# Kernel tuning notes

Measured on AMD Instinct MI355X. Metric: run time of the kernel, lower is better.

## Reference

```python
import jax, jax.numpy as jnp
import numpy as np

B = 64          # graphs per batch
NN = 4096       # nodes per graph (64x64 lattice)
N = B * NN      # total nodes
DEG = 4         # avg degree
E = N * DEG     # total directed edges
DIN, H, L = 1, 128, 64


def setup_inputs() -> dict:
    key = jax.random.key(0)
    ks = jax.random.split(key, 16)
    x = jax.random.normal(ks[0], (N, DIN), dtype=jnp.float32)
    eps = jax.random.normal(ks[1], (B, L), dtype=jnp.float32)
    # per-graph random edges, offset so they never cross graphs
    src = jax.random.randint(ks[2], (E,), 0, NN)
    dst = jax.random.randint(ks[3], (E,), 0, NN)
    off = (jnp.arange(E) // (NN * DEG)) * NN
    edge_index = jnp.stack([src + off, dst + off]).astype(jnp.int32)
    batch = (jnp.arange(N) // NN).astype(jnp.int32)
    s = 0.02
    p = lambda k, shp: s * jax.random.normal(k, shp, dtype=jnp.float32)
    return {
        "x": x, "eps": eps,
        "enc_w1": p(ks[4], (DIN, H)), "enc_b1": jnp.zeros((H,), jnp.float32),
        "enc_w2": p(ks[5], (H, H)),   "enc_b2": jnp.zeros((H,), jnp.float32),
        "mu_w": p(ks[6], (H, L)),     "mu_b": jnp.zeros((L,), jnp.float32),
        "lv_w": p(ks[7], (H, L)),     "lv_b": jnp.zeros((L,), jnp.float32),
        "zn_w": p(ks[8], (L, H)),     "zn_b": jnp.zeros((H,), jnp.float32),
        "dec_w1": p(ks[9], (H, H)),   "dec_b1": jnp.zeros((H,), jnp.float32),
        "dec_w2": p(ks[10], (H, H)),  "dec_b2": jnp.zeros((H,), jnp.float32),
        "out_w": p(ks[11], (H, 1)),   "out_b": jnp.zeros((1,), jnp.float32),
        "edge_index": edge_index, "batch": batch,
    }


def _gcn(h, w, b, row, col, norm, n):
    # PyG GCNConv: xW -> gather at row, scale by sym-norm, scatter-sum at col, + bias
    hw = h @ w
    msg = hw[row] * norm[:, None]
    return jax.ops.segment_sum(msg, col, num_segments=n) + b


def reference(x, eps, enc_w1, enc_b1, enc_w2, enc_b2, mu_w, mu_b, lv_w, lv_b,
              zn_w, zn_b, dec_w1, dec_b1, dec_w2, dec_b2, out_w, out_b,
              edge_index, batch):
    n = x.shape[0]
    b = eps.shape[0]
    nn_ = n // b
    # add self-loops, symmetric GCN normalization (shared by all convs)
    loops = jnp.arange(n, dtype=edge_index.dtype)
    row = jnp.concatenate([edge_index[0], loops])
    col = jnp.concatenate([edge_index[1], loops])
    deg = jax.ops.segment_sum(jnp.ones_like(col, dtype=x.dtype), col, num_segments=n)
    dinv = jnp.where(deg > 0, jax.lax.rsqrt(deg), 0.0)
    norm = dinv[row] * dinv[col]
    h = jax.nn.relu(_gcn(x, enc_w1, enc_b1, row, col, norm, n))
    h = jax.nn.relu(_gcn(h, enc_w2, enc_b2, row, col, norm, n))
    cnt = jax.ops.segment_sum(jnp.ones((n,), x.dtype), batch, num_segments=b)
    hg = jax.ops.segment_sum(h, batch, num_segments=b) / cnt[:, None]
    mu = hg @ mu_w + mu_b
    logvar = hg @ lv_w + lv_b
    # ---- reparameterize ----
    z = mu + jnp.exp(0.5 * logvar) * eps
    zn = z @ zn_w + zn_b          # [B, H]
    hd = zn[batch]                # [N, H]
    hd = jax.nn.relu(_gcn(hd, dec_w1, dec_b1, row, col, norm, n))
    hd = jax.nn.relu(_gcn(hd, dec_w2, dec_b2, row, col, norm, n))
    spin = jnp.tanh(hd @ out_w + out_b)   # [N, 1]
    recon = spin.reshape(b, nn_)
    return (recon, mu, logvar, z)
```

## Files before the change

kernel.cpp:

```cpp
#include <hip/hip_runtime.h>
#include <math.h>

#define NTOT 262144
#define BG   64
#define NNPG 4096
#define ET   1048576
#define EPG  16384
#define HD   128
#define LD   64
#define NSEG 129
#define SLOTPG 28672
#define SLOTCAP (BG*SLOTPG)
#define TN   256

__global__ void __launch_bounds__(1024) k_csr(
    const int* __restrict__ ei, const float* __restrict__ x,
    const float* __restrict__ w1, const float* __restrict__ b1,
    const float* __restrict__ w2,
    int* __restrict__ cnt, int* __restrict__ off, int* __restrict__ csrc,
    float2* __restrict__ axsr,
    float* __restrict__ t1, float* __restrict__ AC1, int* __restrict__ nfp)
{
  __shared__ union {
    struct { int cur[NNPG]; float xs[NNPG]; float dinvs[NNPG];
             float axs[NNPG]; float s1s[NNPG]; int tsum[64]; } c;
    struct { float w2s[HD*HD]; float ts[128], ws[128], bs[128];
             int ks[128], jr[128]; } t;
  } u;
  int tid = threadIdx.x;

  if (blockIdx.x == BG){
    {
      const float4* src = (const float4*)w2;
      float4* dst = (float4*)u.t.w2s;
      for (int idx = tid; idx < HD*HD/4; idx += 1024) dst[idx] = src[idx];
    }
    if (tid < 128){
      float w = w1[tid], b = b1[tid];
      float t; int kind;
      if (w != 0.0f){ t = -b / w; kind = (w > 0.0f) ? 0 : 1; }
      else          { t = INFINITY; kind = 2; }
      u.t.ts[tid] = t; u.t.ks[tid] = kind; u.t.ws[tid] = w; u.t.bs[tid] = b;
      u.t.jr[tid] = -1;
    }
    __syncthreads();
    if (tid == 0){
      int c = 0;
      for (int q = 0; q < 128; q++) c += (u.t.ks[q] != 2) ? 1 : 0;
      nfp[0] = c;
    }
    if (tid < 128){
      int j = tid;
      float t = u.t.ts[j];
      int r = 0;
      for (int q = 0; q < 128; q++){
        if (u.t.ks[q] != 2){
          float tq = u.t.ts[q];
          if (tq < t || (tq == t && q < j)) r++;
        }
      }
      t1[j] = t;
      if (u.t.ks[j] != 2) u.t.jr[r] = j;
    }
    __syncthreads();
    if (tid < 128){
      int k = tid;
      float a = 0.f, c = 0.f;
      for (int q = 0; q < 128; q++){
        int kd = u.t.ks[q];
        bool act = (kd == 1) || (kd == 2 && u.t.bs[q] > 0.0f);
        if (act){ float v = u.t.w2s[q*HD + k]; a = fmaf(u.t.ws[q], v, a); c = fmaf(u.t.bs[q], v, c); }
      }
      int base = (k>>2)*8 + (k&3);
      AC1[base] = a; AC1[base+4] = c;
      for (int s = 0; s < 128; s++){
        int q = u.t.jr[s];
        if (q >= 0){
          float sg = (u.t.ks[q] == 0) ? 1.f : -1.f;
          float v  = u.t.w2s[q*HD + k];
          a = fmaf(sg*u.t.ws[q], v, a);
          c = fmaf(sg*u.t.bs[q], v, c);
        }
        int o = (s+1)*256 + base;
        AC1[o] = a; AC1[o+4] = c;
      }
    }
    return;
  }

  int g = blockIdx.x;
  int gbase = g*NNPG;
  const int4* srcs4 = (const int4*)(ei + g*EPG);
  const int4* dsts4 = (const int4*)(ei + ET + g*EPG);
  int4 S0 = srcs4[0*1024 + tid], S1 = srcs4[1*1024 + tid];
  int4 S2 = srcs4[2*1024 + tid], S3 = srcs4[3*1024 + tid];
  int4 D0 = dsts4[0*1024 + tid], D1 = dsts4[1*1024 + tid];
  int4 D2 = dsts4[2*1024 + tid], D3 = dsts4[3*1024 + tid];
  #pragma unroll
  for (int k = tid; k < NNPG; k += 1024){
    u.c.cur[k] = 0; u.c.axs[k] = 0.f; u.c.s1s[k] = 0.f;
    u.c.xs[k] = x[gbase + k];
  }
  __syncthreads();
  #define CNT4(D_) { atomicAdd(&u.c.cur[D_.x - gbase], 1); atomicAdd(&u.c.cur[D_.y - gbase], 1); \
                     atomicAdd(&u.c.cur[D_.z - gbase], 1); atomicAdd(&u.c.cur[D_.w - gbase], 1); }
  CNT4(D0); CNT4(D1); CNT4(D2); CNT4(D3);
  #undef CNT4
  __syncthreads();
  int n0 = u.c.cur[4*tid+0], n1 = u.c.cur[4*tid+1];
  int n2 = u.c.cur[4*tid+2], n3 = u.c.cur[4*tid+3];
  float di0 = rsqrtf((float)n0 + 1.0f), di1 = rsqrtf((float)n1 + 1.0f);
  float di2 = rsqrtf((float)n2 + 1.0f), di3 = rsqrtf((float)n3 + 1.0f);
  u.c.dinvs[4*tid+0] = di0; u.c.dinvs[4*tid+1] = di1;
  u.c.dinvs[4*tid+2] = di2; u.c.dinvs[4*tid+3] = di3;
  int p0 = (n0+3)&~3, p1 = (n1+3)&~3, p2 = (n2+3)&~3, p3 = (n3+3)&~3;
  int tsum = p0+p1+p2+p3;
  int lane = tid & 63, wv = tid >> 6;
  int incl = tsum;
  #pragma unroll
  for (int dd = 1; dd < 64; dd <<= 1){
    int v = __shfl_up(incl, dd, 64);
    if (lane >= dd) incl += v;
  }
  if (lane == 63) u.c.tsum[wv] = incl;
  __syncthreads();
  if (tid < 64){
    int v = (tid < 16) ? u.c.tsum[tid] : 0;
    int inc2 = v;
    #pragma unroll
    for (int dd = 1; dd < 16; dd <<= 1){
      int t2 = __shfl_up(inc2, dd, 64);
      if (tid >= dd) inc2 += t2;
    }
    if (tid < 16) u.c.tsum[tid] = inc2 - v;
  }
  __syncthreads();
  int tbase = u.c.tsum[wv] + incl - tsum;
  int sbase = g*SLOTPG;
  int o0 = tbase, o1 = o0+p0, o2 = o1+p1, o3 = o2+p2;
  int i0 = gbase + 4*tid;
  *(int4*)(cnt + i0) = make_int4(n0, n1, n2, n3);
  *(int4*)(off + i0) = make_int4(sbase+o0, sbase+o1, sbase+o2, sbase+o3);
  for (int s = n0; s < p0; s++) csrc[sbase+o0+s] = -1;
  for (int s = n1; s < p1; s++) csrc[sbase+o1+s] = -1;
  for (int s = n2; s < p2; s++) csrc[sbase+o2+s] = -1;
  for (int s = n3; s < p3; s++) csrc[sbase+o3+s] = -1;
  u.c.cur[4*tid+0] = o0; u.c.cur[4*tid+1] = o1;
  u.c.cur[4*tid+2] = o2; u.c.cur[4*tid+3] = o3;
  __syncthreads();
  #define PLACE1(s_, d_) { int sl = (s_) - gbase, dl = (d_) - gbase; \
    float v_ = u.c.dinvs[sl]; float xv_ = u.c.xs[sl]; \
    int p_ = atomicAdd(&u.c.cur[dl], 1); \
    csrc[sbase + p_] = (s_); \
    atomicAdd(&u.c.axs[dl], v_*xv_); \
    atomicAdd(&u.c.s1s[dl], v_); }
  #define PLACE4(S_, D_) { PLACE1(S_.x, D_.x); PLACE1(S_.y, D_.y); PLACE1(S_.z, D_.z); PLACE1(S_.w, D_.w); }
  PLACE4(S0, D0); PLACE4(S1, D1); PLACE4(S2, D2); PLACE4(S3, D3);
  #undef PLACE4
  #undef PLACE1
  __syncthreads();
  float ax0 = di0 * (di0 * u.c.xs[4*tid+0] + u.c.axs[4*tid+0]);
  float ax1 = di1 * (di1 * u.c.xs[4*tid+1] + u.c.axs[4*tid+1]);
  float ax2 = di2 * (di2 * u.c.xs[4*tid+2] + u.c.axs[4*tid+2]);
  float ax3 = di3 * (di3 * u.c.xs[4*tid+3] + u.c.axs[4*tid+3]);
  float sr0 = di0 * (di0 + u.c.s1s[4*tid+0]);
  float sr1 = di1 * (di1 + u.c.s1s[4*tid+1]);
  float sr2 = di2 * (di2 + u.c.s1s[4*tid+2]);
  float sr3 = di3 * (di3 + u.c.s1s[4*tid+3]);
  float4* axsr4 = (float4*)axsr;
  int b4 = (gbase >> 1) + tid*2;
  axsr4[b4+0] = make_float4(ax0, sr0, ax1, sr1);
  axsr4[b4+1] = make_float4(ax2, sr2, ax3, sr3);
}

__global__ void k_pack(const float2* __restrict__ axsr,
                       const int* __restrict__ off, const int* __restrict__ cnt,
                       const float* __restrict__ t1,
                       float4* __restrict__ recN, float* __restrict__ srowA){
  __shared__ float ts[128];
  if (threadIdx.x < 128) ts[threadIdx.x] = t1[threadIdx.x];
  __syncthreads();
  int i = blockIdx.x*256 + threadIdx.x;
  int n = cnt[i], eo = off[i];
  float di = rsqrtf((float)n + 1.0f);
  float2 as = axsr[i];
  int sc = 0;
  for (int q = 0; q < 128; q++) sc += (ts[q] < as.x) ? 1 : 0;
  int np = (n + 3) & ~3;
  recN[2*i]   = make_float4(di, di*as.x, di*as.y, __int_as_float(sc));
  recN[2*i+1] = make_float4(__int_as_float(eo), __int_as_float(np), 0.f, 0.f);
  srowA[i] = as.y;
}

__global__ void __launch_bounds__(256) k_enc_agg(
    const float4* __restrict__ recN, const int* __restrict__ csrc,
    const float4* __restrict__ AC, const float* __restrict__ b2,
    const int* __restrict__ nfp, float* __restrict__ hgsum)
{
  __shared__ float4 sS[TN];
  __shared__ float4 sRA[TN];
  __shared__ int sFlag[TN];
  __shared__ float red[256*4];
  int bid = blockIdx.x, g = bid & 63, part = bid >> 6;
  int tid = threadIdx.x, lane = tid & 31, nrow = tid >> 5;
  int base = g*NNPG + part*TN;
  int nf = nfp[0];
  {
    int i = base + tid;
    sRA[tid] = recN[2*i];
    float4 rB = recN[2*i+1];
    int eo = __float_as_int(rB.x), np = __float_as_int(rB.y);
    float swa=0.f, sw=0.f, swaN=0.f, swN=0.f;
    int flag = 0;
    for (int t = 0; t < np; t += 4){
      int4 ss = *(const int4*)(csrc + eo + t);
      #pragma unroll
      for (int uu = 0; uu < 4; uu++){
        int s = (uu==0)?ss.x:(uu==1)?ss.y:(uu==2)?ss.z:ss.w;
        if (s >= 0){
          float4 r = recN[2*s];
          int sb = __float_as_int(r.w);
          swa += r.y; sw += r.x;
          bool isN = (sb == nf) && (sb != 0);
          swaN += isN ? r.y : 0.f;
          swN  += isN ? r.x : 0.f;
          flag |= (sb != 0 && sb != nf) ? 1 : 0;
        }
      }
    }
    sS[tid] = make_float4(swa, sw, swaN, swN);
    sFlag[tid] = flag;
  }
  __syncthreads();
  const float4* q0 = AC + (size_t)lane*2;
  const float4* qn = AC + ((size_t)nf*32 + lane)*2;
  float4 A0 = q0[0], C0 = q0[1], An = qn[0], Cn = qn[1];
  float4 dA = make_float4(An.x-A0.x, An.y-A0.y, An.z-A0.z, An.w-A0.w);
  float4 dC = make_float4(Cn.x-C0.x, Cn.y-C0.y, Cn.z-C0.z, Cn.w-C0.w);
  float4 bb = ((const float4*)b2)[lane];
  float gx=0.f, gy=0.f, gz=0.f, gw=0.f;
  for (int it = 0; it < TN/8; ++it){
    int li = it*8 + nrow;
    int i = base + li;
    float4 rA = sRA[li];
    float accx, accy, accz, accw;
    if (sFlag[li]){
      float4 rB = recN[2*i+1];
      int eo = __float_as_int(rB.x), np = __float_as_int(rB.y);
      float swa=0.f, sw=0.f, swaN=0.f, swN=0.f;
      float mx=0.f, my=0.f, mz=0.f, mw=0.f;
      for (int t = 0; t < np; ++t){
        int s = csrc[eo+t];
        if (s < 0) continue;
        float4 r = recN[2*s];
        int sb = __float_as_int(r.w);
        float v = r.y;
        swa += v; sw += r.x;
        bool isN = (sb == nf) && (sb != 0);
        swaN += isN ? v : 0.f; swN += isN ? r.x : 0.f;
        if (sb != 0 && sb != nf){
          const float4* qm = AC + ((size_t)sb*32 + lane)*2;
          float4 qa = qm[0], qc = qm[1];
          mx = fmaf(v, qa.x-A0.x, fmaf(r.x, qc.x-C0.x, mx));
          my = fmaf(v, qa.y-A0.y, fmaf(r.x, qc.y-C0.y, my));
          mz = fmaf(v, qa.z-A0.z, fmaf(r.x, qc.z-C0.z, mz));
          mw = fmaf(v, qa.w-A0.w, fmaf(r.x, qc.w-C0.w, mw));
        }
      }
      accx = fmaf(swa,A0.x, fmaf(swaN,dA.x, fmaf(sw,C0.x, fmaf(swN,dC.x, mx))));
      accy = fmaf(swa,A0.y, fmaf(swaN,dA.y, fmaf(sw,C0.y, fmaf(swN,dC.y, my))));
      accz = fmaf(swa,A0.z, fmaf(swaN,dA.z, fmaf(sw,C0.z, fmaf(swN,dC.z, mz))));
      accw = fmaf(swa,A0.w, fmaf(swaN,dA.w, fmaf(sw,C0.w, fmaf(swN,dC.w, mw))));
    } else {
      float4 s4 = sS[li];
      accx = fmaf(s4.x,A0.x, fmaf(s4.z,dA.x, fmaf(s4.y,C0.x, s4.w*dC.x)));
      accy = fmaf(s4.x,A0.y, fmaf(s4.z,dA.y, fmaf(s4.y,C0.y, s4.w*dC.y)));
      accz = fmaf(s4.x,A0.z, fmaf(s4.z,dA.z, fmaf(s4.y,C0.z, s4.w*dC.z)));
      accw = fmaf(s4.x,A0.w, fmaf(s4.z,dA.w, fmaf(s4.y,C0.w, s4.w*dC.w)));
    }
    int si = __float_as_int(rA.w);
    bool m0 = (si == 0);
    float4 sa, sc;
    sa.x = m0 ? A0.x : An.x; sa.y = m0 ? A0.y : An.y; sa.z = m0 ? A0.z : An.z; sa.w = m0 ? A0.w : An.w;
    sc.x = m0 ? C0.x : Cn.x; sc.y = m0 ? C0.y : Cn.y; sc.z = m0 ? C0.z : Cn.z; sc.w = m0 ? C0.w : Cn.w;
    if (si != 0 && si != nf){
      const float4* qs = AC + ((size_t)si*32 + lane)*2;
      sa = qs[0]; sc = qs[1];
    }
    float d = rA.x, d2 = d*d, ca = rA.y*d;
    gx += fmaxf(fmaf(d, accx, fmaf(ca, sa.x, d2*sc.x)) + bb.x, 0.f);
    gy += fmaxf(fmaf(d, accy, fmaf(ca, sa.y, d2*sc.y)) + bb.y, 0.f);
    gz += fmaxf(fmaf(d, accz, fmaf(ca, sa.z, d2*sc.z)) + bb.z, 0.f);
    gw += fmaxf(fmaf(d, accw, fmaf(ca, sa.w, d2*sc.w)) + bb.w, 0.f);
  }
  __syncthreads();
  red[tid*4+0] = gx; red[tid*4+1] = gy; red[tid*4+2] = gz; red[tid*4+3] = gw;
  __syncthreads();
  if (nrow == 0){
    float tx=0.f, ty=0.f, tz=0.f, tw=0.f;
    for (int r2 = 0; r2 < 8; r2++){
      int t2 = (r2*32 + lane)*4;
      tx += red[t2]; ty += red[t2+1]; tz += red[t2+2]; tw += red[t2+3];
    }
    atomicAdd(&hgsum[g*HD + lane*4 + 0], tx);
    atomicAdd(&hgsum[g*HD + lane*4 + 1], ty);
    atomicAdd(&hgsum[g*HD + lane*4 + 2], tz);
    atomicAdd(&hgsum[g*HD + lane*4 + 3], tw);
  }
}

__global__ void __launch_bounds__(128) k_small(
    const float* __restrict__ hgsum,
    const float* __restrict__ mu_w, const float* __restrict__ mu_b,
    const float* __restrict__ lv_w, const float* __restrict__ lv_b,
    const float* __restrict__ eps,
    const float* __restrict__ zn_w, const float* __restrict__ zn_b,
    const float* __restrict__ dec_w1, const float* __restrict__ dec_b1,
    float* __restrict__ out_mu, float* __restrict__ out_lv, float* __restrict__ out_z,
    float* __restrict__ t2, float* __restrict__ ushG, int* __restrict__ nf2)
{
  int g = blockIdx.x, tid = threadIdx.x;
  __shared__ float hg[128], zsh[64], znsh[128];
  __shared__ int ks[128];
  hg[tid] = hgsum[g*HD + tid] * (1.0f/4096.0f);
  __syncthreads();
  if (tid < 64){
    int l = tid;
    float m = mu_b[l], v = lv_b[l];
    for (int k = 0; k < HD; k++){
      float hv = hg[k];
      m = fmaf(hv, mu_w[k*LD + l], m);
      v = fmaf(hv, lv_w[k*LD + l], v);
    }
    int o = g*LD + l;
    out_mu[o] = m; out_lv[o] = v;
    float zv = fmaf(expf(0.5f*v), eps[o], m);
    out_z[o] = zv; zsh[l] = zv;
  }
  __syncthreads();
  {
    int k = tid;
    float acc = zn_b[k];
    for (int l = 0; l < LD; l++) acc = fmaf(zsh[l], zn_w[l*HD + k], acc);
    znsh[k] = acc;
  }
  __syncthreads();
  float w;
  {
    int k = tid;
    float acc = 0.f;
    for (int j = 0; j < HD; j++) acc = fmaf(znsh[j], dec_w1[j*HD + k], acc);
    ushG[g*HD + k] = acc;
    w = acc;
  }
  float b = dec_b1[tid];
  float t; int kind;
  if (w != 0.0f){ t = -b / w; kind = (w > 0.0f) ? 0 : 1; }
  else          { t = INFINITY; kind = 2; }
  t2[g*HD + tid] = t; ks[tid] = kind;
  __syncthreads();
  if (tid == 0){
    int c = 0;
    for (int q = 0; q < 128; q++) c += (ks[q] != 2) ? 1 : 0;
    nf2[g] = c;
  }
}

__global__ void k_seg2(const float* __restrict__ t2, const float* __restrict__ srowA,
                       float* __restrict__ recNf, int* __restrict__ segUsed){
  __shared__ float ts[128];
  __shared__ int used[8];
  int tid = threadIdx.x;
  int i = blockIdx.x*256 + tid;
  int g = blockIdx.x >> 4;
  if (tid < 128) ts[tid] = t2[g*HD + tid];
  if (tid < 8) used[tid] = 0;
  __syncthreads();
  float a = srowA[i];
  int sc = 0;
  for (int q = 0; q < 128; q++) sc += (ts[q] < a) ? 1 : 0;
  recNf[(2*i)*4 + 1] = __int_as_float(sc);
  atomicOr(&used[sc>>5], 1u << (sc & 31));
  __syncthreads();
  if (tid < 8 && used[tid]) atomicOr(&segUsed[g*8 + tid], used[tid]);
}

__global__ void __launch_bounds__(128) k_tab2rows(
    const float* __restrict__ ushG, const float* __restrict__ dec_b1,
    const float* __restrict__ w2, const int* __restrict__ segUsed,
    const int* __restrict__ nf2, float* __restrict__ AC2)
{
  __shared__ float w2s[HD*HD];
  __shared__ float ws[128], bs[128], tsh[128];
  __shared__ int ks[128], rr[128];
  int g = blockIdx.x, j = threadIdx.x;
  {
    const float4* src = (const float4*)w2;
    float4* dst = (float4*)w2s;
    #pragma unroll
    for (int idx = 0; idx < HD*HD/4/128; idx++) dst[idx*128 + j] = src[idx*128 + j];
  }
  float w = ushG[g*HD + j], b = dec_b1[j];
  float t; int kind;
  if (w != 0.0f){ t = -b / w; kind = (w > 0.0f) ? 0 : 1; }
  else          { t = INFINITY; kind = 2; }
  ws[j] = w; bs[j] = b; tsh[j] = t; ks[j] = kind;
  __syncthreads();
  int r = 0;
  for (int q = 0; q < 128; q++){
    if (ks[q] != 2){
      float tq = tsh[q];
      if (tq < t || (tq == t && q < j)) r++;
    }
  }
  rr[j] = r;
  __syncthreads();
  int nf = nf2[g];
  float* ACg = AC2 + (size_t)g*NSEG*256;
  int base = (j>>2)*8 + (j&3);
  for (int wd = 0; wd < 5; wd++){
    unsigned m = (unsigned)segUsed[g*8 + wd];
    if (wd == 0) m |= 1u;
    if ((nf >> 5) == wd) m |= 1u << (nf & 31);
    while (m){
      int bit = __ffs(m) - 1;
      m &= m - 1;
      int s = wd*32 + bit;
      float a = 0.f, c = 0.f;
      #pragma unroll 8
      for (int q = 0; q < 128; q++){
        int kd = ks[q];
        bool act = (kd == 0) ? (rr[q] < s) : (kd == 1) ? (rr[q] >= s) : (bs[q] > 0.0f);
        float v = act ? w2s[q*HD + j] : 0.0f;
        a = fmaf(ws[q], v, a); c = fmaf(bs[q], v, c);
      }
      ACg[s*256 + base] = a; ACg[s*256 + base + 4] = c;
    }
  }
}

__global__ void __launch_bounds__(256) k_dec_agg(
    const float4* __restrict__ recN, const int* __restrict__ csrc,
    const float4* __restrict__ AC2, const float* __restrict__ b2,
    const float* __restrict__ ow, const float* __restrict__ ob,
    const int* __restrict__ nf2, float* __restrict__ recon)
{
  __shared__ float4 sS[TN];
  __shared__ float4 sRA[TN];
  __shared__ int sFlag[TN];
  int bid = blockIdx.x, g = bid & 63, part = bid >> 6;
  int tid = threadIdx.x, lane = tid & 31, nrow = tid >> 5;
  int base = g*NNPG + part*TN;
  int nf = nf2[g];
  const float4* AC = AC2 + (size_t)g*NSEG*64;
  {
    int i = base + tid;
    sRA[tid] = recN[2*i];
    float4 rB = recN[2*i+1];
    int eo = __float_as_int(rB.x), np = __float_as_int(rB.y);
    float swa=0.f, sw=0.f, swaN=0.f, swN=0.f;
    int flag = 0;
    for (int t = 0; t < np; t += 4){
      int4 ss = *(const int4*)(csrc + eo + t);
      #pragma unroll
      for (int uu = 0; uu < 4; uu++){
        int s = (uu==0)?ss.x:(uu==1)?ss.y:(uu==2)?ss.z:ss.w;
        if (s >= 0){
          float4 r = recN[2*s];
          int sb = __float_as_int(r.y);
          swa += r.z; sw += r.x;
          bool isN = (sb == nf) && (sb != 0);
          swaN += isN ? r.z : 0.f;
          swN  += isN ? r.x : 0.f;
          flag |= (sb != 0 && sb != nf) ? 1 : 0;
        }
      }
    }
    sS[tid] = make_float4(swa, sw, swaN, swN);
    sFlag[tid] = flag;
  }
  __syncthreads();
  const float4* q0 = AC + (size_t)lane*2;
  const float4* qn = AC + ((size_t)nf*32 + lane)*2;
  float4 A0 = q0[0], C0 = q0[1], An = qn[0], Cn = qn[1];
  float4 dA = make_float4(An.x-A0.x, An.y-A0.y, An.z-A0.z, An.w-A0.w);
  float4 dC = make_float4(Cn.x-C0.x, Cn.y-C0.y, Cn.z-C0.z, Cn.w-C0.w);
  float4 bb  = ((const float4*)b2)[lane];
  float4 owv = ((const float4*)ow)[lane];
  float obv = ob[0];
  for (int it = 0; it < TN/8; ++it){
    int li = it*8 + nrow;
    int i = base + li;
    float4 rA = sRA[li];
    float accx, accy, accz, accw;
    if (sFlag[li]){
      float4 rB = recN[2*i+1];
      int eo = __float_as_int(rB.x), np = __float_as_int(rB.y);
      float swa=0.f, sw=0.f, swaN=0.f, swN=0.f;
      float mx=0.f, my=0.f, mz=0.f, mw=0.f;
      for (int t = 0; t < np; ++t){
        int s = csrc[eo+t];
        if (s < 0) continue;
        float4 r = recN[2*s];
        int sb = __float_as_int(r.y);
        float v = r.z;
        swa += v; sw += r.x;
        bool isN = (sb == nf) && (sb != 0);
        swaN += isN ? v : 0.f; swN += isN ? r.x : 0.f;
        if (sb != 0 && sb != nf){
          const float4* qm = AC + ((size_t)sb*32 + lane)*2;
          float4 qa = qm[0], qc = qm[1];
          mx = fmaf(v, qa.x-A0.x, fmaf(r.x, qc.x-C0.x, mx));
          my = fmaf(v, qa.y-A0.y, fmaf(r.x, qc.y-C0.y, my));
          mz = fmaf(v, qa.z-A0.z, fmaf(r.x, qc.z-C0.z, mz));
          mw = fmaf(v, qa.w-A0.w, fmaf(r.x, qc.w-C0.w, mw));
        }
      }
      accx = fmaf(swa,A0.x, fmaf(swaN,dA.x, fmaf(sw,C0.x, fmaf(swN,dC.x, mx))));
      accy = fmaf(swa,A0.y, fmaf(swaN,dA.y, fmaf(sw,C0.y, fmaf(swN,dC.y, my))));
      accz = fmaf(swa,A0.z, fmaf(swaN,dA.z, fmaf(sw,C0.z, fmaf(swN,dC.z, mz))));
      accw = fmaf(swa,A0.w, fmaf(swaN,dA.w, fmaf(sw,C0.w, fmaf(swN,dC.w, mw))));
    } else {
      float4 s4 = sS[li];
      accx = fmaf(s4.x,A0.x, fmaf(s4.z,dA.x, fmaf(s4.y,C0.x, s4.w*dC.x)));
      accy = fmaf(s4.x,A0.y, fmaf(s4.z,dA.y, fmaf(s4.y,C0.y, s4.w*dC.y)));
      accz = fmaf(s4.x,A0.z, fmaf(s4.z,dA.z, fmaf(s4.y,C0.z, s4.w*dC.z)));
      accw = fmaf(s4.x,A0.w, fmaf(s4.z,dA.w, fmaf(s4.y,C0.w, s4.w*dC.w)));
    }
    int si = __float_as_int(rA.y);
    bool m0 = (si == 0);
    float4 sa, sc;
    sa.x = m0 ? A0.x : An.x; sa.y = m0 ? A0.y : An.y; sa.z = m0 ? A0.z : An.z; sa.w = m0 ? A0.w : An.w;
    sc.x = m0 ? C0.x : Cn.x; sc.y = m0 ? C0.y : Cn.y; sc.z = m0 ? C0.z : Cn.z; sc.w = m0 ? C0.w : Cn.w;
    if (si != 0 && si != nf){
      const float4* qs = AC + ((size_t)si*32 + lane)*2;
      sa = qs[0]; sc = qs[1];
    }
    float d = rA.x, d2 = d*d, ca = rA.z*d;
    float hx = fmaxf(fmaf(d, accx, fmaf(ca, sa.x, d2*sc.x)) + bb.x, 0.f);
    float hy = fmaxf(fmaf(d, accy, fmaf(ca, sa.y, d2*sc.y)) + bb.y, 0.f);
    float hz = fmaxf(fmaf(d, accz, fmaf(ca, sa.z, d2*sc.z)) + bb.z, 0.f);
    float hw = fmaxf(fmaf(d, accw, fmaf(ca, sa.w, d2*sc.w)) + bb.w, 0.f);
    float dsum = hx*owv.x + hy*owv.y + hz*owv.z + hw*owv.w;
    for (int o2 = 16; o2 > 0; o2 >>= 1) dsum += __shfl_down(dsum, o2, 32);
    if (lane == 0) recon[i] = tanhf(dsum + obv);
  }
}

extern "C" void kernel_launch(void* const* d_in, const int* in_sizes, int n_in,
                              void* d_out, int out_size, void* d_ws, size_t ws_size,
                              hipStream_t stream){
  (void)in_sizes; (void)n_in; (void)out_size; (void)ws_size;
  const float* x      = (const float*)d_in[0];
  const float* eps    = (const float*)d_in[1];
  const float* enc_w1 = (const float*)d_in[2];
  const float* enc_b1 = (const float*)d_in[3];
  const float* enc_w2 = (const float*)d_in[4];
  const float* enc_b2 = (const float*)d_in[5];
  const float* mu_w   = (const float*)d_in[6];
  const float* mu_b   = (const float*)d_in[7];
  const float* lv_w   = (const float*)d_in[8];
  const float* lv_b   = (const float*)d_in[9];
  const float* zn_w   = (const float*)d_in[10];
  const float* zn_b   = (const float*)d_in[11];
  const float* dec_w1 = (const float*)d_in[12];
  const float* dec_b1 = (const float*)d_in[13];
  const float* dec_w2 = (const float*)d_in[14];
  const float* dec_b2 = (const float*)d_in[15];
  const float* out_w  = (const float*)d_in[16];
  const float* out_b  = (const float*)d_in[17];
  const int*   ei     = (const int*)d_in[18];

  float* out       = (float*)d_out;
  float* out_recon = out;
  float* out_mu    = out + NTOT;
  float* out_lv    = out_mu + BG*LD;
  float* out_z     = out_lv + BG*LD;

  char* w = (char*)d_ws;
  size_t off_b = 0;
  auto alloc = [&](size_t bytes)->void*{
    void* p = w + off_b;
    off_b += (bytes + 255) & ~(size_t)255;
    return p;
  };
  int*    cnt    = (int*)   alloc((size_t)NTOT*4);
  int*    eoP    = (int*)   alloc((size_t)NTOT*4);
  int*    csrc   = (int*)   alloc((size_t)SLOTCAP*4);
  float2* axsr   = (float2*)alloc((size_t)NTOT*8);
  float4* recN   = (float4*)alloc(((size_t)NTOT*2 + 32)*16);
  float*  srowA  = (float*) alloc((size_t)NTOT*4);
  float*  t1     = (float*) alloc(128*4);
  int*    nf1    = (int*)   alloc(256);
  int*    nf2    = (int*)   alloc(BG*4);
  int*    segU   = (int*)   alloc(BG*8*4);
  float*  ushG   = (float*) alloc((size_t)BG*HD*4);
  float*  AC1    = (float*) alloc((size_t)NSEG*256*4);
  float*  hgsum  = (float*) alloc((size_t)BG*HD*4);
  float*  t2     = (float*) alloc((size_t)BG*HD*4);
  float*  AC2    = (float*) alloc((size_t)BG*NSEG*256*4);

  hipMemsetAsync(hgsum, 0, (size_t)BG*HD*4, stream);
  hipMemsetAsync(segU,  0, (size_t)BG*8*4, stream);

  k_csr<<<BG+1, 1024, 0, stream>>>(ei, x, enc_w1, enc_b1, enc_w2,
                                   cnt, eoP, csrc, axsr, t1, AC1, nf1);

  k_pack<<<NTOT/256, 256, 0, stream>>>(axsr, eoP, cnt, t1, recN, srowA);

  k_enc_agg<<<1024, 256, 0, stream>>>(recN, csrc, (const float4*)AC1, enc_b2, nf1, hgsum);

  k_small<<<BG, 128, 0, stream>>>(hgsum, mu_w, mu_b, lv_w, lv_b, eps,
                                  zn_w, zn_b, dec_w1, dec_b1,
                                  out_mu, out_lv, out_z, t2, ushG, nf2);

  k_seg2<<<NTOT/256, 256, 0, stream>>>(t2, srowA, (float*)recN, segU);

  k_tab2rows<<<BG, 128, 0, stream>>>(ushG, dec_b1, dec_w2, segU, nf2, AC2);

  k_dec_agg<<<1024, 256, 0, stream>>>(recN, csrc, (const float4*)AC2,
                                      dec_b2, out_w, out_b, nf2, out_recon);
}
```

Baseline: 182.1 us.

## Split per-graph CSR build into count/scan/place kernels with global atomics

Replaces the single 65-block CSR construction kernel, one 1024-thread block per graph using LDS atomics, with three kernels. k_count uses 256 blocks and global atomics to count in-degrees, k_scan does a per-graph prefix sum, and k_place uses 256 blocks plus a table block to scatter edges and accumulate the first-layer aggregates with global atomics. Blocks are swizzled so the four blocks of one graph share an XCD. The goal is to occupy more CUs than 65 blocks can. The cost is two extra launches, a memset, and slower global atomics in place of LDS atomics.

Result: slower. 339.7 us (+86.5%).

```diff
diff --git a/kernel.cpp b/kernel.cpp
--- a/kernel.cpp
+++ b/kernel.cpp
@@ -13,107 +13,33 @@
 #define SLOTCAP (BG*SLOTPG)
 #define TN   256
 
-__global__ void __launch_bounds__(1024) k_csr(
-    const int* __restrict__ ei, const float* __restrict__ x,
-    const float* __restrict__ w1, const float* __restrict__ b1,
-    const float* __restrict__ w2,
-    int* __restrict__ cnt, int* __restrict__ off, int* __restrict__ csrc,
-    float2* __restrict__ axsr,
-    float* __restrict__ t1, float* __restrict__ AC1, int* __restrict__ nfp)
-{
-  __shared__ union {
-    struct { int cur[NNPG]; float xs[NNPG]; float dinvs[NNPG];
-             float axs[NNPG]; float s1s[NNPG]; int tsum[64]; } c;
-    struct { float w2s[HD*HD]; float ts[128], ws[128], bs[128];
-             int ks[128], jr[128]; } t;
-  } u;
+__device__ __forceinline__ void swz(int b, int& g, int& j){
+  int xcd = b & 7, q = b >> 3;
+  g = (q >> 2)*8 + xcd;
+  j = q & 3;
+}
+
+__global__ void __launch_bounds__(1024) k_count(const int* __restrict__ ei,
+                                                int* __restrict__ cnt,
+                                                float2* __restrict__ acc){
+  int g, j; swz(blockIdx.x, g, j);
   int tid = threadIdx.x;
-
-  if (blockIdx.x == BG){
-    {
-      const float4* src = (const float4*)w2;
-      float4* dst = (float4*)u.t.w2s;
-      for (int idx = tid; idx < HD*HD/4; idx += 1024) dst[idx] = src[idx];
-    }
-    if (tid < 128){
-      float w = w1[tid], b = b1[tid];
-      float t; int kind;
-      if (w != 0.0f){ t = -b / w; kind = (w > 0.0f) ? 0 : 1; }
-      else          { t = INFINITY; kind = 2; }
-      u.t.ts[tid] = t; u.t.ks[tid] = kind; u.t.ws[tid] = w; u.t.bs[tid] = b;
-      u.t.jr[tid] = -1;
-    }
-    __syncthreads();
-    if (tid == 0){
-      int c = 0;
-      for (int q = 0; q < 128; q++) c += (u.t.ks[q] != 2) ? 1 : 0;
-      nfp[0] = c;
-    }
-    if (tid < 128){
-      int j = tid;
-      float t = u.t.ts[j];
-      int r = 0;
-      for (int q = 0; q < 128; q++){
-        if (u.t.ks[q] != 2){
-          float tq = u.t.ts[q];
-          if (tq < t || (tq == t && q < j)) r++;
-        }
-      }
-      t1[j] = t;
-      if (u.t.ks[j] != 2) u.t.jr[r] = j;
-    }
-    __syncthreads();
-    if (tid < 128){
-      int k = tid;
-      float a = 0.f, c = 0.f;
-      for (int q = 0; q < 128; q++){
-        int kd = u.t.ks[q];
-        bool act = (kd == 1) || (kd == 2 && u.t.bs[q] > 0.0f);
-        if (act){ float v = u.t.w2s[q*HD + k]; a = fmaf(u.t.ws[q], v, a); c = fmaf(u.t.bs[q], v, c); }
-      }
-      int base = (k>>2)*8 + (k&3);
-      AC1[base] = a; AC1[base+4] = c;
-      for (int s = 0; s < 128; s++){
-        int q = u.t.jr[s];
-        if (q >= 0){
-          float sg = (u.t.ks[q] == 0) ? 1.f : -1.f;
-          float v  = u.t.w2s[q*HD + k];
-          a = fmaf(sg*u.t.ws[q], v, a);
-          c = fmaf(sg*u.t.bs[q], v, c);
-        }
-        int o = (s+1)*256 + base;
-        AC1[o] = a; AC1[o+4] = c;
-      }
-    }
-    return;
-  }
-
-  int g = blockIdx.x;
-  int gbase = g*NNPG;
-  const int4* srcs4 = (const int4*)(ei + g*EPG);
-  const int4* dsts4 = (const int4*)(ei + ET + g*EPG);
-  int4 S0 = srcs4[0*1024 + tid], S1 = srcs4[1*1024 + tid];
-  int4 S2 = srcs4[2*1024 + tid], S3 = srcs4[3*1024 + tid];
-  int4 D0 = dsts4[0*1024 + tid], D1 = dsts4[1*1024 + tid];
-  int4 D2 = dsts4[2*1024 + tid], D3 = dsts4[3*1024 + tid];
-  #pragma unroll
-  for (int k = tid; k < NNPG; k += 1024){
-    u.c.cur[k] = 0; u.c.axs[k] = 0.f; u.c.s1s[k] = 0.f;
-    u.c.xs[k] = x[gbase + k];
-  }
-  __syncthreads();
-  #define CNT4(D_) { atomicAdd(&u.c.cur[D_.x - gbase], 1); atomicAdd(&u.c.cur[D_.y - gbase], 1); \
-                     atomicAdd(&u.c.cur[D_.z - gbase], 1); atomicAdd(&u.c.cur[D_.w - gbase], 1); }
-  CNT4(D0); CNT4(D1); CNT4(D2); CNT4(D3);
-  #undef CNT4
-  __syncthreads();
-  int n0 = u.c.cur[4*tid+0], n1 = u.c.cur[4*tid+1];
-  int n2 = u.c.cur[4*tid+2], n3 = u.c.cur[4*tid+3];
-  float di0 = rsqrtf((float)n0 + 1.0f), di1 = rsqrtf((float)n1 + 1.0f);
-  float di2 = rsqrtf((float)n2 + 1.0f), di3 = rsqrtf((float)n3 + 1.0f);
-  u.c.dinvs[4*tid+0] = di0; u.c.dinvs[4*tid+1] = di1;
-  u.c.dinvs[4*tid+2] = di2; u.c.dinvs[4*tid+3] = di3;
-  int p0 = (n0+3)&~3, p1 = (n1+3)&~3, p2 = (n2+3)&~3, p3 = (n3+3)&~3;
+  acc[blockIdx.x*1024 + tid] = make_float2(0.f, 0.f);
+  const int4* dsts4 = (const int4*)(ei + ET + g*EPG + j*4096);
+  int4 D = dsts4[tid];
+  atomicAdd(&cnt[D.x], 1); atomicAdd(&cnt[D.y], 1);
+  atomicAdd(&cnt[D.z], 1); atomicAdd(&cnt[D.w], 1);
+}
+
+__global__ void __launch_bounds__(1024) k_scan(const int* __restrict__ cnt,
+                                               const float* __restrict__ x,
+                                               int* __restrict__ off, int* __restrict__ cursor,
+                                               int* __restrict__ csrc, float2* __restrict__ xd){
+  __shared__ int tsums[16];
+  int g = blockIdx.x, tid = threadIdx.x, gbase = g*NNPG;
+  int4 n4 = *(const int4*)(cnt + gbase + 4*tid);
+  float4 xv = *(const float4*)(x + gbase + 4*tid);
+  int p0 = (n4.x+3)&~3, p1 = (n4.y+3)&~3, p2 = (n4.z+3)&~3, p3 = (n4.w+3)&~3;
   int tsum = p0+p1+p2+p3;
   int lane = tid & 63, wv = tid >> 6;
   int incl = tsum;
@@ -122,58 +48,120 @@
     int v = __shfl_up(incl, dd, 64);
     if (lane >= dd) incl += v;
   }
-  if (lane == 63) u.c.tsum[wv] = incl;
+  if (lane == 63) tsums[wv] = incl;
   __syncthreads();
   if (tid < 64){
-    int v = (tid < 16) ? u.c.tsum[tid] : 0;
+    int v = (tid < 16) ? tsums[tid] : 0;
     int inc2 = v;
     #pragma unroll
     for (int dd = 1; dd < 16; dd <<= 1){
       int t2 = __shfl_up(inc2, dd, 64);
       if (tid >= dd) inc2 += t2;
     }
-    if (tid < 16) u.c.tsum[tid] = inc2 - v;
-  }
-  __syncthreads();
-  int tbase = u.c.tsum[wv] + incl - tsum;
-  int sbase = g*SLOTPG;
-  int o0 = tbase, o1 = o0+p0, o2 = o1+p1, o3 = o2+p2;
+    if (tid < 16) tsums[tid] = inc2 - v;
+  }
+  __syncthreads();
+  int tbase = tsums[wv] + incl - tsum;
+  int o0 = g*SLOTPG + tbase, o1 = o0+p0, o2 = o1+p1, o3 = o2+p2;
   int i0 = gbase + 4*tid;
-  *(int4*)(cnt + i0) = make_int4(n0, n1, n2, n3);
-  *(int4*)(off + i0) = make_int4(sbase+o0, sbase+o1, sbase+o2, sbase+o3);
-  for (int s = n0; s < p0; s++) csrc[sbase+o0+s] = -1;
-  for (int s = n1; s < p1; s++) csrc[sbase+o1+s] = -1;
-  for (int s = n2; s < p2; s++) csrc[sbase+o2+s] = -1;
-  for (int s = n3; s < p3; s++) csrc[sbase+o3+s] = -1;
-  u.c.cur[4*tid+0] = o0; u.c.cur[4*tid+1] = o1;
-  u.c.cur[4*tid+2] = o2; u.c.cur[4*tid+3] = o3;
-  __syncthreads();
-  #define PLACE1(s_, d_) { int sl = (s_) - gbase, dl = (d_) - gbase; \
-    float v_ = u.c.dinvs[sl]; float xv_ = u.c.xs[sl]; \
-    int p_ = atomicAdd(&u.c.cur[dl], 1); \
-    csrc[sbase + p_] = (s_); \
-    atomicAdd(&u.c.axs[dl], v_*xv_); \
-    atomicAdd(&u.c.s1s[dl], v_); }
-  #define PLACE4(S_, D_) { PLACE1(S_.x, D_.x); PLACE1(S_.y, D_.y); PLACE1(S_.z, D_.z); PLACE1(S_.w, D_.w); }
-  PLACE4(S0, D0); PLACE4(S1, D1); PLACE4(S2, D2); PLACE4(S3, D3);
-  #undef PLACE4
+  *(int4*)(off + i0)    = make_int4(o0, o1, o2, o3);
+  *(int4*)(cursor + i0) = make_int4(o0, o1, o2, o3);
+  float d0 = rsqrtf((float)n4.x + 1.0f), d1 = rsqrtf((float)n4.y + 1.0f);
+  float d2 = rsqrtf((float)n4.z + 1.0f), d3 = rsqrtf((float)n4.w + 1.0f);
+  float4* xd4 = (float4*)xd;
+  xd4[i0/2 + 0] = make_float4(xv.x, d0, xv.y, d1);
+  xd4[i0/2 + 1] = make_float4(xv.z, d2, xv.w, d3);
+  for (int s = n4.x; s < p0; s++) csrc[o0+s] = -1;
+  for (int s = n4.y; s < p1; s++) csrc[o1+s] = -1;
+  for (int s = n4.z; s < p2; s++) csrc[o2+s] = -1;
+  for (int s = n4.w; s < p3; s++) csrc[o3+s] = -1;
+}
+
+__global__ void __launch_bounds__(1024) k_place(
+    const int* __restrict__ ei, const float2* __restrict__ xd,
+    int* __restrict__ cursor, int* __restrict__ csrc, float2* __restrict__ acc,
+    const float* __restrict__ w1, const float* __restrict__ b1,
+    const float* __restrict__ w2,
+    float* __restrict__ t1, float* __restrict__ AC1, int* __restrict__ nfp)
+{
+  __shared__ float w2s[HD*HD];
+  __shared__ float tss[128], wss[128], bss[128];
+  __shared__ int kss[128], jrs[128];
+  int tid = threadIdx.x;
+  if (blockIdx.x == 256){
+    {
+      const float4* src = (const float4*)w2;
+      float4* dst = (float4*)w2s;
+      for (int idx = tid; idx < HD*HD/4; idx += 1024) dst[idx] = src[idx];
+    }
+    if (tid < 128){
+      float w = w1[tid], b = b1[tid];
+      float t; int kind;
+      if (w != 0.0f){ t = -b / w; kind = (w > 0.0f) ? 0 : 1; }
+      else          { t = INFINITY; kind = 2; }
+      tss[tid] = t; kss[tid] = kind; wss[tid] = w; bss[tid] = b;
+      jrs[tid] = -1;
+    }
+    __syncthreads();
+    if (tid == 0){
+      int c = 0;
+      for (int q = 0; q < 128; q++) c += (kss[q] != 2) ? 1 : 0;
+      nfp[0] = c;
+    }
+    if (tid < 128){
+      int j = tid;
+      float t = tss[j];
+      int r = 0;
+      for (int q = 0; q < 128; q++){
+        if (kss[q] != 2){
+          float tq = tss[q];
+          if (tq < t || (tq == t && q < j)) r++;
+        }
+      }
+      t1[j] = t;
+      if (kss[j] != 2) jrs[r] = j;
+    }
+    __syncthreads();
+    if (tid < 128){
+      int k = tid;
+      float a = 0.f, c = 0.f;
+      for (int q = 0; q < 128; q++){
+        int kd = kss[q];
+        bool act = (kd == 1) || (kd == 2 && bss[q] > 0.0f);
+        if (act){ float v = w2s[q*HD + k]; a = fmaf(wss[q], v, a); c = fmaf(bss[q], v, c); }
+      }
+      int base = (k>>2)*8 + (k&3);
+      AC1[base] = a; AC1[base+4] = c;
+      for (int s = 0; s < 128; s++){
+        int q = jrs[s];
+        if (q >= 0){
+          float sg = (kss[q] == 0) ? 1.f : -1.f;
+          float v  = w2s[q*HD + k];
+          a = fmaf(sg*wss[q], v, a);
+          c = fmaf(sg*bss[q], v, c);
+        }
+        int o = (s+1)*256 + base;
+        AC1[o] = a; AC1[o+4] = c;
+      }
+    }
+    return;
+  }
+  int g, j; swz(blockIdx.x, g, j);
+  const int4* srcs4 = (const int4*)(ei + g*EPG + j*4096);
+  const int4* dsts4 = (const int4*)(ei + ET + g*EPG + j*4096);
+  int4 S = srcs4[tid], D = dsts4[tid];
+  float* accf = (float*)acc;
+  #define PLACE1(s_, d_) { \
+    float2 sd_ = xd[s_]; \
+    int p_ = atomicAdd(&cursor[d_], 1); \
+    csrc[p_] = (s_); \
+    atomicAdd(&accf[2*(d_)],   sd_.y * sd_.x); \
+    atomicAdd(&accf[2*(d_)+1], sd_.y); }
+  PLACE1(S.x, D.x); PLACE1(S.y, D.y); PLACE1(S.z, D.z); PLACE1(S.w, D.w);
   #undef PLACE1
-  __syncthreads();
-  float ax0 = di0 * (di0 * u.c.xs[4*tid+0] + u.c.axs[4*tid+0]);
-  float ax1 = di1 * (di1 * u.c.xs[4*tid+1] + u.c.axs[4*tid+1]);
-  float ax2 = di2 * (di2 * u.c.xs[4*tid+2] + u.c.axs[4*tid+2]);
-  float ax3 = di3 * (di3 * u.c.xs[4*tid+3] + u.c.axs[4*tid+3]);
-  float sr0 = di0 * (di0 + u.c.s1s[4*tid+0]);
-  float sr1 = di1 * (di1 + u.c.s1s[4*tid+1]);
-  float sr2 = di2 * (di2 + u.c.s1s[4*tid+2]);
-  float sr3 = di3 * (di3 + u.c.s1s[4*tid+3]);
-  float4* axsr4 = (float4*)axsr;
-  int b4 = (gbase >> 1) + tid*2;
-  axsr4[b4+0] = make_float4(ax0, sr0, ax1, sr1);
-  axsr4[b4+1] = make_float4(ax2, sr2, ax3, sr3);
-}
-
-__global__ void k_pack(const float2* __restrict__ axsr,
+}
+
+__global__ void k_pack(const float2* __restrict__ xd, const float2* __restrict__ acc,
                        const int* __restrict__ off, const int* __restrict__ cnt,
                        const float* __restrict__ t1,
                        float4* __restrict__ recN, float* __restrict__ srowA){
@@ -183,13 +171,16 @@
   int i = blockIdx.x*256 + threadIdx.x;
   int n = cnt[i], eo = off[i];
   float di = rsqrtf((float)n + 1.0f);
-  float2 as = axsr[i];
+  float2 xdv = xd[i];
+  float2 a2 = acc[i];
+  float ax = di * (di * xdv.x + a2.x);
+  float sr = di * (di + a2.y);
   int sc = 0;
-  for (int q = 0; q < 128; q++) sc += (ts[q] < as.x) ? 1 : 0;
+  for (int q = 0; q < 128; q++) sc += (ts[q] < ax) ? 1 : 0;
   int np = (n + 3) & ~3;
-  recN[2*i]   = make_float4(di, di*as.x, di*as.y, __int_as_float(sc));
+  recN[2*i]   = make_float4(di, di*ax, di*sr, __int_as_float(sc));
   recN[2*i+1] = make_float4(__int_as_float(eo), __int_as_float(np), 0.f, 0.f);
-  srowA[i] = as.y;
+  srowA[i] = sr;
 }
 
 __global__ void __launch_bounds__(256) k_enc_agg(
@@ -586,8 +577,10 @@
   };
   int*    cnt    = (int*)   alloc((size_t)NTOT*4);
   int*    eoP    = (int*)   alloc((size_t)NTOT*4);
+  int*    cursor = (int*)   alloc((size_t)NTOT*4);
   int*    csrc   = (int*)   alloc((size_t)SLOTCAP*4);
-  float2* axsr   = (float2*)alloc((size_t)NTOT*8);
+  float2* xd     = (float2*)alloc((size_t)NTOT*8);
+  float2* acc    = (float2*)alloc((size_t)NTOT*8);
   float4* recN   = (float4*)alloc(((size_t)NTOT*2 + 32)*16);
   float*  srowA  = (float*) alloc((size_t)NTOT*4);
   float*  t1     = (float*) alloc(128*4);
@@ -600,13 +593,16 @@
   float*  t2     = (float*) alloc((size_t)BG*HD*4);
   float*  AC2    = (float*) alloc((size_t)BG*NSEG*256*4);
 
+  hipMemsetAsync(cnt,   0, (size_t)NTOT*4, stream);
   hipMemsetAsync(hgsum, 0, (size_t)BG*HD*4, stream);
   hipMemsetAsync(segU,  0, (size_t)BG*8*4, stream);
 
-  k_csr<<<BG+1, 1024, 0, stream>>>(ei, x, enc_w1, enc_b1, enc_w2,
-                                   cnt, eoP, csrc, axsr, t1, AC1, nf1);
-
-  k_pack<<<NTOT/256, 256, 0, stream>>>(axsr, eoP, cnt, t1, recN, srowA);
+  k_count<<<256, 1024, 0, stream>>>(ei, cnt, acc);
+  k_scan <<<BG, 1024, 0, stream>>>(cnt, x, eoP, cursor, csrc, xd);
+  k_place<<<257, 1024, 0, stream>>>(ei, xd, cursor, csrc, acc,
+                                    enc_w1, enc_b1, enc_w2, t1, AC1, nf1);
+
+  k_pack<<<NTOT/256, 256, 0, stream>>>(xd, acc, eoP, cnt, t1, recN, srowA);
 
   k_enc_agg<<<1024, 256, 0, stream>>>(recN, csrc, (const float4*)AC1, enc_b2, nf1, hgsum);
 
```
